# Kernel tuning notes

Measured on AMD Instinct MI355X. Metric: run time of the kernel, lower is better.

Reference implementation:

```python
import jax, jax.numpy as jnp
import numpy as np

TEMP = 0.5
WEIGHT = (0.4, 0.3, 0.3)


def _l2norm(x):
    n = jnp.linalg.norm(x, axis=-1, keepdims=True)
    return x / jnp.maximum(n, 1e-12)


def _forward(st_i, st_j, car_i, car_j, pl_i, pl_j, gt_labels,
             cen_st, cen_car, cen_pl, conc):
    w = jnp.asarray(WEIGHT, dtype=st_i.dtype)[:, None, None]  # [3,1,1]
    feats = [jnp.concatenate([_l2norm(a), _l2norm(b)], axis=0)
             for a, b in ((st_i, st_j), (car_i, car_j), (pl_i, pl_j))]  # each [N,D]
    sims = jnp.stack([f @ f.T for f in feats])  # [3,N,N]
    wmask = jnp.where(sims == 0, jnp.zeros_like(w), w)
    wsim = (sims * wmask).sum(0) / (wmask.sum(0) + 1e-12)  # [N,N]
    e = jnp.exp(wsim / TEMP)
    N = e.shape[0]
    B = N // 2
    idx = jnp.arange(N)
    pos = e[idx, (idx + B) % N]  # positive_mask gather: one positive per row
    # negative_mask excludes diagonal and the positive -> row sum minus both
    neg_sum = e.sum(-1) - e[idx, idx] - pos
    loss = (-jnp.log(pos / (pos + neg_sum))).mean()

    # prototype branch: gt_labels covers all C clusters, unique set == arange(C)
    labels = gt_labels[:, 0]  # [N]
    C = cen_st.shape[0]
    k = jnp.arange(C - 1)
    neg_ids = k[None, :] + (k[None, :] >= labels[:, None]).astype(k.dtype)  # sorted ids != label
    proto_ids = jnp.concatenate([labels[:, None], neg_ids], axis=1)  # [N,C], col 0 = positive
    logits = jnp.stack([
        jnp.take_along_axis(f @ c.T, proto_ids, axis=1)
        for f, c in zip(feats, (cen_st, cen_car, cen_pl))])  # [3,N,C]
    temp_proto = conc[:, proto_ids]  # [3,N,C]
    logits = logits / (temp_proto + 1e-12)
    w2 = jnp.where((temp_proto == 0) | (logits == 0), jnp.zeros_like(w), w)
    logits_w = (logits * w2).sum(0) / (w2.sum(0) + 1e-12)  # [N,C]
    # CrossEntropyLoss(mean) with target class 0 for every row
    loss_proto = (-jax.nn.log_softmax(logits_w, axis=-1)[:, 0]).mean()
    return loss + loss_proto


def setup_inputs() -> dict:
    key = jax.random.key(0)
    ks = jax.random.split(key, 12)
    B, D, C = 2048, 128, 512
    N = 2 * B
    inp = {}
    names = ['st_feat_i', 'st_feat_j', 'car_feat_i', 'car_feat_j',
             'plate_feat_i', 'plate_feat_j']
    for i, nm in enumerate(names):
        inp[nm] = jax.random.normal(ks[i], (B, D), dtype=jnp.float32)
    # labels covering all C clusters so torch.unique(gt_labels) == arange(C)
    labels = jnp.tile(jnp.arange(C, dtype=jnp.int32), N // C)
    labels = jax.random.permutation(ks[6], labels)
    inp['gt_labels'] = labels[:, None]
    inp['st_centroids'] = jax.random.normal(ks[7], (C, D), dtype=jnp.float32)
    inp['car_centroids'] = jax.random.normal(ks[8], (C, D), dtype=jnp.float32)
    inp['plate_centroids'] = jax.random.normal(ks[9], (C, D), dtype=jnp.float32)
    inp['concentration'] = jax.random.uniform(ks[10], (3, C), dtype=jnp.float32,
                                              minval=0.1, maxval=1.0)
    return inp


def reference(st_feat_i, st_feat_j, car_feat_i, car_feat_j,
              plate_feat_i, plate_feat_j, gt_labels,
              st_centroids, car_centroids, plate_centroids, concentration):
    return _forward(st_feat_i, st_feat_j, car_feat_i, car_feat_j,
                    plate_feat_i, plate_feat_j, gt_labels,
                    st_centroids, car_centroids, plate_centroids, concentration)
```

## Files before the change

kernel.cpp:

```cpp
#include <hip/hip_runtime.h>
#include <hip/hip_bf16.h>
#include <math.h>

#define BB 2048
#define NN 4096
#define DD 128
#define CC 512
#define NSIM 528
#define NPROTO 128

typedef __attribute__((ext_vector_type(8))) short bf16x8;
typedef __attribute__((ext_vector_type(4))) float f32x4;

__global__ __launch_bounds__(512) void k_normprep(
    const float* __restrict__ si, const float* __restrict__ sj,
    const float* __restrict__ ci, const float* __restrict__ cj,
    const float* __restrict__ pi, const float* __restrict__ pj,
    const float* __restrict__ cst, const float* __restrict__ cca,
    const float* __restrict__ cpl, const float* __restrict__ conc,
    __hip_bfloat16* __restrict__ fbf, __hip_bfloat16* __restrict__ cbf,
    float* __restrict__ rowsum) {
  const int m   = blockIdx.y;
  const int tid = threadIdx.x;
  const int w   = tid >> 6;
  const int t   = tid & 63;
  const float sqw = (m == 0) ? 0.632455532033676f : 0.547722557505166f;

  if (m == 2 && blockIdx.x < 2) {
    const int i = (blockIdx.x * 512 + tid) * 4;
    *(float4*)(rowsum + i) = make_float4(0.f, 0.f, 0.f, 0.f);
  }

  if (blockIdx.x < NN / 8) {
    const int row = blockIdx.x * 8 + w;
    const float* src;
    if (m == 0)      src = (row < BB) ? si : sj;
    else if (m == 1) src = (row < BB) ? ci : cj;
    else             src = (row < BB) ? pi : pj;
    const int r = (row < BB) ? row : row - BB;
    float2 v = ((const float2*)(src + (size_t)r * DD))[t];
    float ss = v.x * v.x + v.y * v.y;
    #pragma unroll
    for (int k = 32; k >= 1; k >>= 1) ss += __shfl_xor(ss, k);
    const float inv = sqw / fmaxf(sqrtf(ss), 1e-12f);
    __hip_bfloat16* db = fbf + (size_t)m * NN * DD + (size_t)row * DD;
    db[2 * t]     = __float2bfloat16(v.x * inv);
    db[2 * t + 1] = __float2bfloat16(v.y * inv);
  } else {
    const int crow = (blockIdx.x - NN / 8) * 8 + w;
    const float* src = (m == 0) ? cst : (m == 1) ? cca : cpl;
    const float sc = sqw / (conc[m * CC + crow] + 1e-12f);
    float2 v = ((const float2*)(src + (size_t)crow * DD))[t];
    __hip_bfloat16* db = cbf + (size_t)m * CC * DD + (size_t)crow * DD;
    db[2 * t]     = __float2bfloat16(v.x * sc);
    db[2 * t + 1] = __float2bfloat16(v.y * sc);
  }
}

__global__ __launch_bounds__(256, 3) void k_main(const __hip_bfloat16* __restrict__ fbf,
                                                 const __hip_bfloat16* __restrict__ cbf,
                                                 const int* __restrict__ labels,
                                                 float* __restrict__ rowsum,
                                                 float* __restrict__ pos_e,
                                                 float* __restrict__ diag_e,
                                                 float* __restrict__ pmax_g,
                                                 float* __restrict__ psum_g,
                                                 float* __restrict__ zl_g) {
  __shared__ bf16x8 As[1024];
  __shared__ bf16x8 Bs[1024];

  const int tid  = threadIdx.x;
  const int lane = tid & 63;
  const int wid  = tid >> 6;
  const int l15  = lane & 15;
  const int kg   = lane >> 4;

  if (blockIdx.x < NSIM) {
    int tB = blockIdx.x;
    int by = 0;
    while (tB >= 32 - by) { tB -= 32 - by; ++by; }
    const int bx = by + tB;
    const bool diag = (by == bx);
    const int rowBase = by * 128;
    const int colBase = bx * 128;

    const int wr = wid >> 1, wc = wid & 1;
    const int srow = tid >> 3;
    const int kc   = tid & 7;
    const int sc   = kc ^ (srow & 7);

    f32x4 acc[4][4] = {};
    bf16x8 ra[4], rb[4];

    {
      const __hip_bfloat16* F = fbf;
      #pragma unroll
      for (int q = 0; q < 4; ++q) {
        ra[q] = *(const bf16x8*)(F + (size_t)(rowBase + q * 32 + srow) * DD + kc * 8);
        if (!diag)
          rb[q] = *(const bf16x8*)(F + (size_t)(colBase + q * 32 + srow) * DD + kc * 8);
      }
    }

    for (int t = 0; t < 6; ++t) {
      #pragma unroll
      for (int q = 0; q < 4; ++q) {
        As[(q * 32 + srow) * 8 + sc] = ra[q];
        if (!diag) Bs[(q * 32 + srow) * 8 + sc] = rb[q];
      }
      __syncthreads();

      if (t < 5) {
        const __hip_bfloat16* F = fbf + (size_t)((t + 1) >> 1) * NN * DD + ((t + 1) & 1) * 64;
        #pragma unroll
        for (int q = 0; q < 4; ++q) {
          ra[q] = *(const bf16x8*)(F + (size_t)(rowBase + q * 32 + srow) * DD + kc * 8);
          if (!diag)
            rb[q] = *(const bf16x8*)(F + (size_t)(colBase + q * 32 + srow) * DD + kc * 8);
        }
      }

      const bf16x8* Bsrc = diag ? As : Bs;
      #pragma unroll
      for (int ks2 = 0; ks2 < 2; ++ks2) {
        bf16x8 a[4], b[4];
        const int ch = (ks2 * 4 + kg) ^ (l15 & 7);
        #pragma unroll
        for (int ti = 0; ti < 4; ++ti)
          a[ti] = As[(wr * 64 + ti * 16 + l15) * 8 + ch];
        #pragma unroll
        for (int tj = 0; tj < 4; ++tj)
          b[tj] = Bsrc[(wc * 64 + tj * 16 + l15) * 8 + ch];
        #pragma unroll
        for (int ti = 0; ti < 4; ++ti)
          #pragma unroll
          for (int tj = 0; tj < 4; ++tj)
            acc[ti][tj] = __builtin_amdgcn_mfma_f32_16x16x32_bf16(a[ti], b[tj], acc[ti][tj], 0, 0, 0);
      }
      __syncthreads();
    }

    float csum[4] = {0.f, 0.f, 0.f, 0.f};
    #pragma unroll
    for (int ti = 0; ti < 4; ++ti) {
      #pragma unroll
      for (int j = 0; j < 4; ++j) {
        const int i = rowBase + wr * 64 + ti * 16 + kg * 4 + j;
        float rsum = 0.f;
        #pragma unroll
        for (int tj = 0; tj < 4; ++tj) {
          const int jcol = colBase + wc * 64 + tj * 16 + l15;
          const float e = expf(2.0f * acc[ti][tj][j]);
          rsum += e;
          csum[tj] += e;
          if (diag) {
            if (jcol == i) diag_e[i] = e;
          } else if (jcol == ((i + BB) & (NN - 1))) {
            pos_e[i] = e;
            pos_e[jcol] = e;
          }
        }
        #pragma unroll
        for (int msk = 8; msk >= 1; msk >>= 1) rsum += __shfl_xor(rsum, msk);
        if (l15 == 0) atomicAdd(&rowsum[i], rsum);
      }
    }
    if (!diag) {
      #pragma unroll
      for (int tj = 0; tj < 4; ++tj) {
        float v = csum[tj];
        v += __shfl_xor(v, 16);
        v += __shfl_xor(v, 32);
        if (lane < 16) atomicAdd(&rowsum[colBase + wc * 64 + tj * 16 + l15], v);
      }
    }
  } else {
    float* wmaxs = (float*)As;
    float* wsums = wmaxs + 256;
    int*   slab  = (int*)(wsums + 256);

    const int bidp = blockIdx.x - NSIM;
    const int half = bidp & 1;
    const int row0 = (bidp >> 1) * 64;
    const int cbase = half * 256 + wid * 64;

    if (tid < 64) slab[tid] = labels[row0 + tid];
    __syncthreads();

    f32x4 acc[4][4] = {};
    #pragma unroll
    for (int ks = 0; ks < 12; ++ks) {
      const int koff = (ks & 3) * 32 + kg * 8;
      const __hip_bfloat16* F  = fbf + (size_t)(ks >> 2) * NN * DD + koff;
      const __hip_bfloat16* Cm = cbf + (size_t)(ks >> 2) * CC * DD + koff;
      bf16x8 af[4], bfr[4];
      #pragma unroll
      for (int ti = 0; ti < 4; ++ti)
        af[ti] = *(const bf16x8*)(F + (size_t)(row0 + ti * 16 + l15) * DD);
      #pragma unroll
      for (int tj = 0; tj < 4; ++tj)
        bfr[tj] = *(const bf16x8*)(Cm + (size_t)(cbase + tj * 16 + l15) * DD);
      #pragma unroll
      for (int ti = 0; ti < 4; ++ti)
        #pragma unroll
        for (int tj = 0; tj < 4; ++tj)
          acc[ti][tj] = __builtin_amdgcn_mfma_f32_16x16x32_bf16(af[ti], bfr[tj], acc[ti][tj], 0, 0, 0);
    }

    #pragma unroll
    for (int ti = 0; ti < 4; ++ti) {
      #pragma unroll
      for (int j = 0; j < 4; ++j) {
        const int r = ti * 16 + kg * 4 + j;
        #pragma unroll
        for (int tj = 0; tj < 4; ++tj) {
          const int c = cbase + tj * 16 + l15;
          if (c == slab[r]) zl_g[row0 + r] = acc[ti][tj][j];
        }
      }
    }

    #pragma unroll
    for (int ti = 0; ti < 4; ++ti) {
      #pragma unroll
      for (int j = 0; j < 4; ++j) {
        const int r = ti * 16 + kg * 4 + j;
        float mx = acc[ti][0][j];
        #pragma unroll
        for (int tj = 1; tj < 4; ++tj) mx = fmaxf(mx, acc[ti][tj][j]);
        #pragma unroll
        for (int msk = 8; msk >= 1; msk >>= 1) mx = fmaxf(mx, __shfl_xor(mx, msk));
        if (l15 == 0) wmaxs[wid * 64 + r] = mx;
      }
    }
    __syncthreads();

    #pragma unroll
    for (int ti = 0; ti < 4; ++ti) {
      #pragma unroll
      for (int j = 0; j < 4; ++j) {
        const int r = ti * 16 + kg * 4 + j;
        const float bmx = fmaxf(fmaxf(wmaxs[0 * 64 + r], wmaxs[1 * 64 + r]),
                                fmaxf(wmaxs[2 * 64 + r], wmaxs[3 * 64 + r]));
        float se = 0.f;
        #pragma unroll
        for (int tj = 0; tj < 4; ++tj) se += expf(acc[ti][tj][j] - bmx);
        #pragma unroll
        for (int msk = 8; msk >= 1; msk >>= 1) se += __shfl_xor(se, msk);
        if (l15 == 0) wsums[wid * 64 + r] = se;
      }
    }
    __syncthreads();

    if (tid < 64) {
      const int r = tid;
      const float bmx = fmaxf(fmaxf(wmaxs[0 * 64 + r], wmaxs[1 * 64 + r]),
                              fmaxf(wmaxs[2 * 64 + r], wmaxs[3 * 64 + r]));
      const float s = wsums[0 * 64 + r] + wsums[1 * 64 + r] +
                      wsums[2 * 64 + r] + wsums[3 * 64 + r];
      pmax_g[(size_t)half * NN + row0 + r] = bmx;
      psum_g[(size_t)half * NN + row0 + r] = s;
    }
  }
}

__global__ void k_final(const float* __restrict__ rowsum, const float* __restrict__ pos_e,
                        const float* __restrict__ diag_e, const float* __restrict__ pmax_g,
                        const float* __restrict__ psum_g, const float* __restrict__ zl_g,
                        float* __restrict__ out) {
  __shared__ float redA[4], redB[4];
  const int tid = threadIdx.x;
  float sa = 0.f, sb = 0.f;
  for (int i = tid; i < NN; i += 256) {
    sa += logf(rowsum[i] - diag_e[i]) - logf(pos_e[i]);
    const float m0 = pmax_g[i], m1 = pmax_g[NN + i];
    const float M = fmaxf(m0, m1);
    const float s = psum_g[i] * expf(m0 - M) + psum_g[NN + i] * expf(m1 - M);
    sb += M + logf(s) - zl_g[i];
  }
  const int lane = tid & 63, wv = tid >> 6;
  #pragma unroll
  for (int k = 32; k >= 1; k >>= 1) { sa += __shfl_xor(sa, k); sb += __shfl_xor(sb, k); }
  if (lane == 0) { redA[wv] = sa; redB[wv] = sb; }
  __syncthreads();
  if (tid == 0) {
    const float la = redA[0] + redA[1] + redA[2] + redA[3];
    const float lb = redB[0] + redB[1] + redB[2] + redB[3];
    out[0] = la / (float)NN + lb / (float)NN;
  }
}

extern "C" void kernel_launch(void* const* d_in, const int* in_sizes, int n_in,
                              void* d_out, int out_size, void* d_ws, size_t ws_size,
                              hipStream_t stream) {
  (void)in_sizes; (void)n_in; (void)out_size; (void)ws_size;
  const float* si  = (const float*)d_in[0];
  const float* sj  = (const float*)d_in[1];
  const float* ci  = (const float*)d_in[2];
  const float* cj  = (const float*)d_in[3];
  const float* pi  = (const float*)d_in[4];
  const float* pj  = (const float*)d_in[5];
  const int*   lab = (const int*)d_in[6];
  const float* cst = (const float*)d_in[7];
  const float* cca = (const float*)d_in[8];
  const float* cpl = (const float*)d_in[9];
  const float* cnc = (const float*)d_in[10];

  float* ws     = (float*)d_ws;
  float* rowsum = ws;
  float* pos_e  = rowsum + NN;
  float* diag_e = pos_e + NN;
  float* pmax_g = diag_e + NN;
  float* psum_g = pmax_g + 2 * NN;
  float* zl_g   = psum_g + 2 * NN;
  __hip_bfloat16* fbf = (__hip_bfloat16*)(zl_g + NN);
  __hip_bfloat16* cbf = fbf + (size_t)3 * NN * DD;

  k_normprep<<<dim3(NN / 8 + CC / 8, 3), 512, 0, stream>>>(si, sj, ci, cj, pi, pj,
                                                           cst, cca, cpl, cnc, fbf, cbf, rowsum);
  k_main<<<NSIM + NPROTO, 256, 0, stream>>>(fbf, cbf, lab, rowsum, pos_e, diag_e,
                                            pmax_g, psum_g, zl_g);
  k_final<<<1, 256, 0, stream>>>(rowsum, pos_e, diag_e, pmax_g, psum_g, zl_g, (float*)d_out);
}
```

Measured before the change: 118.9 us.

## Load GEMM tiles directly into LDS, merge normprep grid, use fast exp/log

Replaces the register-staged prefetch of bf16 feature tiles with global_load_lds direct-to-LDS transfers, keeping the XOR swizzle via the source address. The normalization kernel now handles all three modalities per block instead of a 3-wide grid. Precise expf/logf are replaced with __expf/__logf intrinsics. The direct loads save VGPRs and LDS store instructions but drop the explicit overlap of next-tile loads with MFMA work; the fast intrinsics slightly reduce accuracy.

```diff
diff --git a/kernel.cpp b/kernel.cpp
--- a/kernel.cpp
+++ b/kernel.cpp
@@ -11,6 +11,9 @@
 
 typedef __attribute__((ext_vector_type(8))) short bf16x8;
 typedef __attribute__((ext_vector_type(4))) float f32x4;
+
+#define LDS_PTR(p) ((__attribute__((address_space(3))) uint32_t*)(p))
+#define GLB_PTR(p) ((const __attribute__((address_space(1))) uint32_t*)(p))
 
 __global__ __launch_bounds__(512) void k_normprep(
     const float* __restrict__ si, const float* __restrict__ sj,
@@ -20,40 +23,46 @@
     const float* __restrict__ cpl, const float* __restrict__ conc,
     __hip_bfloat16* __restrict__ fbf, __hip_bfloat16* __restrict__ cbf,
     float* __restrict__ rowsum) {
-  const int m   = blockIdx.y;
   const int tid = threadIdx.x;
   const int w   = tid >> 6;
   const int t   = tid & 63;
-  const float sqw = (m == 0) ? 0.632455532033676f : 0.547722557505166f;
-
-  if (m == 2 && blockIdx.x < 2) {
+
+  if (blockIdx.x < 2) {
     const int i = (blockIdx.x * 512 + tid) * 4;
     *(float4*)(rowsum + i) = make_float4(0.f, 0.f, 0.f, 0.f);
   }
 
   if (blockIdx.x < NN / 8) {
     const int row = blockIdx.x * 8 + w;
-    const float* src;
-    if (m == 0)      src = (row < BB) ? si : sj;
-    else if (m == 1) src = (row < BB) ? ci : cj;
-    else             src = (row < BB) ? pi : pj;
     const int r = (row < BB) ? row : row - BB;
-    float2 v = ((const float2*)(src + (size_t)r * DD))[t];
-    float ss = v.x * v.x + v.y * v.y;
-    #pragma unroll
-    for (int k = 32; k >= 1; k >>= 1) ss += __shfl_xor(ss, k);
-    const float inv = sqw / fmaxf(sqrtf(ss), 1e-12f);
-    __hip_bfloat16* db = fbf + (size_t)m * NN * DD + (size_t)row * DD;
-    db[2 * t]     = __float2bfloat16(v.x * inv);
-    db[2 * t + 1] = __float2bfloat16(v.y * inv);
+    #pragma unroll
+    for (int m = 0; m < 3; ++m) {
+      const float* src;
+      if (m == 0)      src = (row < BB) ? si : sj;
+      else if (m == 1) src = (row < BB) ? ci : cj;
+      else             src = (row < BB) ? pi : pj;
+      const float sqw = (m == 0) ? 0.632455532033676f : 0.547722557505166f;
+      float2 v = ((const float2*)(src + (size_t)r * DD))[t];
+      float ss = v.x * v.x + v.y * v.y;
+      #pragma unroll
+      for (int k = 32; k >= 1; k >>= 1) ss += __shfl_xor(ss, k);
+      const float inv = sqw / fmaxf(sqrtf(ss), 1e-12f);
+      __hip_bfloat16* db = fbf + (size_t)m * NN * DD + (size_t)row * DD;
+      db[2 * t]     = __float2bfloat16(v.x * inv);
+      db[2 * t + 1] = __float2bfloat16(v.y * inv);
+    }
   } else {
     const int crow = (blockIdx.x - NN / 8) * 8 + w;
-    const float* src = (m == 0) ? cst : (m == 1) ? cca : cpl;
-    const float sc = sqw / (conc[m * CC + crow] + 1e-12f);
-    float2 v = ((const float2*)(src + (size_t)crow * DD))[t];
-    __hip_bfloat16* db = cbf + (size_t)m * CC * DD + (size_t)crow * DD;
-    db[2 * t]     = __float2bfloat16(v.x * sc);
-    db[2 * t + 1] = __float2bfloat16(v.y * sc);
+    #pragma unroll
+    for (int m = 0; m < 3; ++m) {
+      const float* src = (m == 0) ? cst : (m == 1) ? cca : cpl;
+      const float sqw = (m == 0) ? 0.632455532033676f : 0.547722557505166f;
+      const float sc = sqw / (conc[m * CC + crow] + 1e-12f);
+      float2 v = ((const float2*)(src + (size_t)crow * DD))[t];
+      __hip_bfloat16* db = cbf + (size_t)m * CC * DD + (size_t)crow * DD;
+      db[2 * t]     = __float2bfloat16(v.x * sc);
+      db[2 * t + 1] = __float2bfloat16(v.y * sc);
+    }
   }
 }
 
@@ -85,40 +94,25 @@
     const int colBase = bx * 128;
 
     const int wr = wid >> 1, wc = wid & 1;
-    const int srow = tid >> 3;
-    const int kc   = tid & 7;
-    const int sc   = kc ^ (srow & 7);
+    const int rl = lane >> 3;
+    const int kc = (lane & 7) ^ rl;
 
     f32x4 acc[4][4] = {};
-    bf16x8 ra[4], rb[4];
-
-    {
-      const __hip_bfloat16* F = fbf;
+
+    for (int t = 0; t < 6; ++t) {
+      const __hip_bfloat16* F = fbf + (size_t)(t >> 1) * NN * DD + (t & 1) * 64;
       #pragma unroll
       for (int q = 0; q < 4; ++q) {
-        ra[q] = *(const bf16x8*)(F + (size_t)(rowBase + q * 32 + srow) * DD + kc * 8);
+        const int row = q * 32 + wid * 8 + rl;
+        __builtin_amdgcn_global_load_lds(
+            GLB_PTR(F + (size_t)(rowBase + row) * DD + kc * 8),
+            LDS_PTR(&As[q * 256 + wid * 64]), 16, 0, 0);
         if (!diag)
-          rb[q] = *(const bf16x8*)(F + (size_t)(colBase + q * 32 + srow) * DD + kc * 8);
-      }
-    }
-
-    for (int t = 0; t < 6; ++t) {
-      #pragma unroll
-      for (int q = 0; q < 4; ++q) {
-        As[(q * 32 + srow) * 8 + sc] = ra[q];
-        if (!diag) Bs[(q * 32 + srow) * 8 + sc] = rb[q];
+          __builtin_amdgcn_global_load_lds(
+              GLB_PTR(F + (size_t)(colBase + row) * DD + kc * 8),
+              LDS_PTR(&Bs[q * 256 + wid * 64]), 16, 0, 0);
       }
       __syncthreads();
-
-      if (t < 5) {
-        const __hip_bfloat16* F = fbf + (size_t)((t + 1) >> 1) * NN * DD + ((t + 1) & 1) * 64;
-        #pragma unroll
-        for (int q = 0; q < 4; ++q) {
-          ra[q] = *(const bf16x8*)(F + (size_t)(rowBase + q * 32 + srow) * DD + kc * 8);
-          if (!diag)
-            rb[q] = *(const bf16x8*)(F + (size_t)(colBase + q * 32 + srow) * DD + kc * 8);
-        }
-      }
 
       const bf16x8* Bsrc = diag ? As : Bs;
       #pragma unroll
@@ -137,7 +131,7 @@
           for (int tj = 0; tj < 4; ++tj)
             acc[ti][tj] = __builtin_amdgcn_mfma_f32_16x16x32_bf16(a[ti], b[tj], acc[ti][tj], 0, 0, 0);
       }
-      __syncthreads();
+      if (t < 5) __syncthreads();
     }
 
     float csum[4] = {0.f, 0.f, 0.f, 0.f};
@@ -150,7 +144,7 @@
         #pragma unroll
         for (int tj = 0; tj < 4; ++tj) {
           const int jcol = colBase + wc * 64 + tj * 16 + l15;
-          const float e = expf(2.0f * acc[ti][tj][j]);
+          const float e = __expf(2.0f * acc[ti][tj][j]);
           rsum += e;
           csum[tj] += e;
           if (diag) {
@@ -244,7 +238,7 @@
                                 fmaxf(wmaxs[2 * 64 + r], wmaxs[3 * 64 + r]));
         float se = 0.f;
         #pragma unroll
-        for (int tj = 0; tj < 4; ++tj) se += expf(acc[ti][tj][j] - bmx);
+        for (int tj = 0; tj < 4; ++tj) se += __expf(acc[ti][tj][j] - bmx);
         #pragma unroll
         for (int msk = 8; msk >= 1; msk >>= 1) se += __shfl_xor(se, msk);
         if (l15 == 0) wsums[wid * 64 + r] = se;
@@ -272,11 +266,11 @@
   const int tid = threadIdx.x;
   float sa = 0.f, sb = 0.f;
   for (int i = tid; i < NN; i += 256) {
-    sa += logf(rowsum[i] - diag_e[i]) - logf(pos_e[i]);
+    sa += __logf(rowsum[i] - diag_e[i]) - __logf(pos_e[i]);
     const float m0 = pmax_g[i], m1 = pmax_g[NN + i];
     const float M = fmaxf(m0, m1);
-    const float s = psum_g[i] * expf(m0 - M) + psum_g[NN + i] * expf(m1 - M);
-    sb += M + logf(s) - zl_g[i];
+    const float s = psum_g[i] * __expf(m0 - M) + psum_g[NN + i] * __expf(m1 - M);
+    sb += M + __logf(s) - zl_g[i];
   }
   const int lane = tid & 63, wv = tid >> 6;
   #pragma unroll
@@ -316,8 +310,8 @@
   __hip_bfloat16* fbf = (__hip_bfloat16*)(zl_g + NN);
   __hip_bfloat16* cbf = fbf + (size_t)3 * NN * DD;
 
-  k_normprep<<<dim3(NN / 8 + CC / 8, 3), 512, 0, stream>>>(si, sj, ci, cj, pi, pj,
-                                                           cst, cca, cpl, cnc, fbf, cbf, rowsum);
+  k_normprep<<<NN / 8 + CC / 8, 512, 0, stream>>>(si, sj, ci, cj, pi, pj,
+                                                  cst, cca, cpl, cnc, fbf, cbf, rowsum);
   k_main<<<NSIM + NPROTO, 256, 0, stream>>>(fbf, cbf, lab, rowsum, pos_e, diag_e,
                                             pmax_g, psum_g, zl_g);
   k_final<<<1, 256, 0, stream>>>(rowsum, pos_e, diag_e, pmax_g, psum_g, zl_g, (float*)d_out);
```

New measurement: 119.0 us. Within noise of the previous version (+0.1%).
